# Optimization experiments

Measured on AMD Instinct MI355X. Metric: run time of the kernel, lower is better.

Reference implementation:

```python
import jax, jax.numpy as jnp
import numpy as np

GAMMAS = jnp.array([2.7, 2.1, 2.4, 2.0, 3.0, 2.9, 3.0, 2.5, 2.1, 2.6, 2.0, 2.1, 2.7, 2.4, 2.2], dtype=jnp.float32)

B, NCLS, H, W = 32, 15, 256, 256
K, CREG = 500, 2


def setup_inputs() -> dict:
    key = jax.random.key(0)
    ks = jax.random.split(key, 6)
    pred = jax.random.uniform(ks[0], (B, NCLS, H, W), dtype=jnp.float32)
    gt = jax.random.uniform(ks[1], (B, NCLS, H, W), dtype=jnp.float32)
    output = jax.random.normal(ks[2], (B, CREG, H, W), dtype=jnp.float32)
    mask = jax.random.randint(ks[3], (B, K), 0, 2, dtype=jnp.int32)
    ind = jax.random.randint(ks[4], (B, K), 0, H * W)
    target = jax.random.normal(ks[5], (B, K, CREG), dtype=jnp.float32)
    inde = jax.random.randint(jax.random.fold_in(key, 7), (B, K, 3), 0, 15)
    return {"pred": pred, "gt": gt, "output": output, "mask": mask,
            "ind": ind, "target": target, "inde": inde}


def _forward(pred, gt, output, mask, ind, target, inde):
    b, c_out = output.shape[0], output.shape[1]
    k = ind.shape[1]
    # _tranpose_and_gather_feat: [B,C,H,W] -> [B,HW,C], gather along dim 1
    feat = jnp.transpose(output, (0, 2, 3, 1)).reshape(b, -1, c_out)
    pre = jnp.take_along_axis(feat, ind[:, :, None].astype(jnp.int32), axis=1)  # [B,K,C]

    d = pre - target
    ad = jnp.abs(d)
    huber = jnp.where(ad < 1.0, 0.5 * d * d, ad - 0.5)
    l_bk = huber.mean(axis=2)  # [B,K]

    pos_mask = mask.astype(bool)
    factor = jnp.arctan(l_bk) * (2.0 / jnp.pi)
    vals = jnp.where(pos_mask, factor, 1.0).reshape(-1)

    b_idx = jnp.broadcast_to(jnp.arange(b)[:, None], (b, k)).reshape(-1)
    ch = inde[..., 0].reshape(-1)
    yy = inde[..., 1].reshape(-1)
    xx = inde[..., 2].reshape(-1)
    # in-place multiplicative scatter; torch's pred_uni aliases pred so the
    # modified tensor is used for BOTH pred_cat and pred_cat_uni below
    pred_mod = pred.at[b_idx, ch, yy, xx].multiply(vals)

    # loss is overwritten each loop iteration in the original: only the LAST
    # positive's smooth-L1 loss survives (0 if no positives)
    flat_m = pos_mask.reshape(-1)
    flat_l = l_bk.reshape(-1)
    last = jnp.max(jnp.where(flat_m, jnp.arange(flat_m.shape[0]), -1))
    loss0 = jnp.where(last >= 0, flat_l[jnp.clip(last, 0)], 0.0)

    # focal term, vectorized over the 15 class channels
    eps = 1e-12
    g = GAMMAS[None, :, None, None]
    pos_inds = (gt == 1.0).astype(pred.dtype)
    neg_inds = (gt < 1.0).astype(pred.dtype)
    neg_weights = jnp.power(1.0 - gt, 4)
    pos_loss = jnp.log(pred_mod + eps) * jnp.power(1.0 - pred_mod, g) * pos_inds
    neg_loss = jnp.log(1.0 - pred_mod + eps) * jnp.power(pred_mod, g) * neg_weights * neg_inds
    per_ch = jnp.sum(pos_loss + neg_loss, axis=(0, 2, 3))  # [15]
    loss = loss0 - jnp.sum(per_ch * GAMMAS * 0.5)

    num_pos = pos_inds.sum()
    return jnp.where(num_pos == 0, loss, loss / num_pos)


def reference(pred, gt, output, mask, ind, target, inde):
    return _forward(pred, gt, output, mask, ind, target, inde)
```

## Files before the change

### kernel.cpp

```cpp
#include <hip/hip_runtime.h>
#include <math.h>

#define BB 32
#define NCLS 15
#define HH 256
#define WW 256
#define KK 500
#define HW (HH*WW)
#define NELEM (BB*NCLS*HW)
#define N4 (NELEM/4)
#define NM (BB*NCLS*16*16)
#define BK (BB*KK)

#define MG 1536
#define MT 256
#define SPAN (MG*MT)
#define MITER 5

typedef float v4f __attribute__((ext_vector_type(4)));

#define OFF_LBK 4
#define OFF_M   16384

__constant__ float c_gammas[15] = {2.7f,2.1f,2.4f,2.0f,3.0f,2.9f,3.0f,2.5f,
                                   2.1f,2.6f,2.0f,2.1f,2.7f,2.4f,2.2f};

#define EXP2F(x) __builtin_amdgcn_exp2f(x)
#define LOG2F(x) __builtin_amdgcn_logf(x)
#define LN2 0.69314718055994530942f

__device__ __forceinline__ float elem(float p, float g, float gam, float& np) {
    float t    = 1.0f - g;
    float t2   = t * t;
    float negw = (g < 1.0f) ? t2 * t2 : 0.0f;
    float pw   = EXP2F(gam * LOG2F(p));
    float v    = (LN2 * LOG2F(1.0f - p + 1e-12f)) * pw * negw;
    if (g == 1.0f) {
        np += 1.0f;
        v += (LN2 * LOG2F(p + 1e-12f)) * EXP2F(gam * LOG2F(1.0f - p));
    }
    return v;
}

__device__ __forceinline__ float quad(v4f p, v4f g, int i, float& np) {
    int c = ((unsigned)i >> 14) % (unsigned)NCLS;
    float gam = c_gammas[c];
    return gam * (elem(p.x, g.x, gam, np) + elem(p.y, g.y, gam, np)
                + elem(p.z, g.z, gam, np) + elem(p.w, g.w, gam, np));
}

__device__ __forceinline__ float blockReduceSum(float v) {
    __shared__ float sh[4];
    #pragma unroll
    for (int o = 32; o > 0; o >>= 1) v += __shfl_down(v, o);
    int lane = threadIdx.x & 63, w = threadIdx.x >> 6;
    if (lane == 0) sh[w] = v;
    __syncthreads();
    float r = 0.0f;
    if (threadIdx.x == 0) r = sh[0] + sh[1] + sh[2] + sh[3];
    __syncthreads();
    return r;
}

__global__ __launch_bounds__(256) void k_init(float* ws) {
    int i = blockIdx.x * blockDim.x + threadIdx.x;
    if (i == 0) {
        ws[0] = 0.0f;
        ws[1] = 0.0f;
        ((int*)ws)[2] = -1;
        ((int*)ws)[3] = 0;
    }
    if (i < NM) ws[OFF_M + i] = 1.0f;
}

__global__ __launch_bounds__(256) void k_bk(const float* __restrict__ output,
                                            const int*   __restrict__ mask,
                                            const int*   __restrict__ ind,
                                            const float* __restrict__ target,
                                            const int*   __restrict__ inde,
                                            float* ws) {
    int t = blockIdx.x * blockDim.x + threadIdx.x;
    int lastv = -1;
    if (t < BK) {
        int b = t / KK;
        int pos = ind[t];
        const float* ob = output + (size_t)b * 2 * HW;
        float p0 = ob[pos];
        float p1 = ob[HW + pos];
        float d0 = p0 - target[t*2 + 0];
        float d1 = p1 - target[t*2 + 1];
        float a0 = fabsf(d0), a1 = fabsf(d1);
        float h0 = (a0 < 1.0f) ? 0.5f*d0*d0 : a0 - 0.5f;
        float h1 = (a1 < 1.0f) ? 0.5f*d1*d1 : a1 - 0.5f;
        float l  = 0.5f * (h0 + h1);
        ws[OFF_LBK + t] = l;
        if (mask[t] != 0) {
            lastv = t;
            float factor = atanf(l) * 0.63661977236758134308f;
            int ch = inde[t*3 + 0];
            int yy = inde[t*3 + 1];
            int xx = inde[t*3 + 2];
            int mi = ((b*NCLS + ch)*16 + yy)*16 + xx;
            unsigned int* addr = (unsigned int*)(ws + OFF_M + mi);
            unsigned int old = *addr, assumed;
            do {
                assumed = old;
                float nv = __uint_as_float(assumed) * factor;
                old = atomicCAS(addr, assumed, __float_as_uint(nv));
            } while (old != assumed);
        }
    }
    __shared__ int shm[4];
    int v = lastv;
    #pragma unroll
    for (int o = 32; o > 0; o >>= 1) v = max(v, __shfl_down(v, o));
    int lane = threadIdx.x & 63, w = threadIdx.x >> 6;
    if (lane == 0) shm[w] = v;
    __syncthreads();
    if (threadIdx.x == 0) {
        int m = max(max(shm[0], shm[1]), max(shm[2], shm[3]));
        if (m >= 0) atomicMax(((int*)ws) + 2, m);
    }
}

__global__ __launch_bounds__(256) void k_main(const v4f* __restrict__ pred,
                                              const v4f* __restrict__ gt,
                                              float* ws) {
    int t = blockIdx.x * MT + threadIdx.x;
    float acc = 0.0f, np = 0.0f;
    #pragma unroll 1
    for (int k = 0; k < MITER; ++k) {
        int i0 = t + k * 4 * SPAN;
        v4f p0 = __builtin_nontemporal_load(pred + i0);
        v4f p1 = __builtin_nontemporal_load(pred + i0 + SPAN);
        v4f p2 = __builtin_nontemporal_load(pred + i0 + 2*SPAN);
        v4f p3 = __builtin_nontemporal_load(pred + i0 + 3*SPAN);
        v4f g0 = __builtin_nontemporal_load(gt + i0);
        v4f g1 = __builtin_nontemporal_load(gt + i0 + SPAN);
        v4f g2 = __builtin_nontemporal_load(gt + i0 + 2*SPAN);
        v4f g3 = __builtin_nontemporal_load(gt + i0 + 3*SPAN);
        acc += quad(p0, g0, i0,          np);
        acc += quad(p1, g1, i0 + SPAN,   np);
        acc += quad(p2, g2, i0 + 2*SPAN, np);
        acc += quad(p3, g3, i0 + 3*SPAN, np);
    }
    float bs = blockReduceSum(acc);
    if (threadIdx.x == 0 && bs != 0.0f) atomicAdd(&ws[0], bs);
    float bn = blockReduceSum(np);
    if (threadIdx.x == 0 && bn != 0.0f) atomicAdd(&ws[1], bn);
}

__global__ __launch_bounds__(256) void k_corr(const float* __restrict__ pred,
                                              const float* __restrict__ gt,
                                              float* ws, float* out) {
    int i = blockIdx.x * blockDim.x + threadIdx.x;
    float acc = 0.0f, dummy = 0.0f;
    float m = ws[OFF_M + i];
    if (m != 1.0f) {
        int x  = i & 15;
        int y  = (i >> 4) & 15;
        int bc = i >> 8;
        int c  = bc % NCLS;
        size_t off = ((size_t)bc << 16) + (size_t)(y * WW + x);
        float p = pred[off];
        float g = gt[off];
        float gam = c_gammas[c];
        acc = gam * (elem(p * m, g, gam, dummy) - elem(p, g, gam, dummy));
    }
    float bs = blockReduceSum(acc);
    if (threadIdx.x == 0) {
        if (bs != 0.0f) atomicAdd(&ws[0], bs);
        __threadfence();
        int done = atomicAdd(((int*)ws) + 3, 1);
        if (done == gridDim.x - 1) {
            float S  = atomicAdd(&ws[0], 0.0f);
            float np = atomicAdd(&ws[1], 0.0f);
            int last = ((volatile int*)ws)[2];
            float loss0 = (last >= 0) ? ws[OFF_LBK + last] : 0.0f;
            float loss = loss0 - 0.5f * S;
            out[0] = (np == 0.0f) ? loss : loss / np;
        }
    }
}

extern "C" void kernel_launch(void* const* d_in, const int* in_sizes, int n_in,
                              void* d_out, int out_size, void* d_ws, size_t ws_size,
                              hipStream_t stream) {
    const float* pred   = (const float*)d_in[0];
    const float* gt     = (const float*)d_in[1];
    const float* output = (const float*)d_in[2];
    const int*   mask   = (const int*)d_in[3];
    const int*   ind    = (const int*)d_in[4];
    const float* target = (const float*)d_in[5];
    const int*   inde   = (const int*)d_in[6];
    float* ws  = (float*)d_ws;
    float* out = (float*)d_out;

    k_init<<<(NM + 255)/256, 256, 0, stream>>>(ws);
    k_bk  <<<(BK + 255)/256, 256, 0, stream>>>(output, mask, ind, target, inde, ws);
    k_main<<<MG, MT, 0, stream>>>((const v4f*)pred, (const v4f*)gt, ws);
    k_corr<<<NM/256, 256, 0, stream>>>(pred, gt, ws, out);
}
```

Baseline: 289.8 us.

## Fuse regression gather kernel into focal-loss streaming kernel with per-block channel mapping

Merges the per-(b,k) smooth-L1/scatter kernel into the main focal-loss reduction kernel. Each block handles 9 (b,k) entries in its first threads, then streams a quarter of one (b,c) slab. Because the channel is fixed per block, the gamma lookup is hoisted out of the loop. This removes one kernel launch and its tail, but puts the atomic scatter work on the critical path of some waves.

```diff
diff --git a/kernel.cpp b/kernel.cpp
--- a/kernel.cpp
+++ b/kernel.cpp
@@ -12,10 +12,11 @@
 #define NM (BB*NCLS*16*16)
 #define BK (BB*KK)
 
-#define MG 1536
-#define MT 256
-#define SPAN (MG*MT)
-#define MITER 5
+#define FG 1920
+#define FT 256
+#define SLAB4 16384
+#define QUART 4096
+#define BKPB 9
 
 typedef float v4f __attribute__((ext_vector_type(4)));
 
@@ -42,11 +43,9 @@
     return v;
 }
 
-__device__ __forceinline__ float quad(v4f p, v4f g, int i, float& np) {
-    int c = ((unsigned)i >> 14) % (unsigned)NCLS;
-    float gam = c_gammas[c];
-    return gam * (elem(p.x, g.x, gam, np) + elem(p.y, g.y, gam, np)
-                + elem(p.z, g.z, gam, np) + elem(p.w, g.w, gam, np));
+__device__ __forceinline__ float elem4(v4f p, v4f g, float gam, float& np) {
+    return elem(p.x, g.x, gam, np) + elem(p.y, g.y, gam, np)
+         + elem(p.z, g.z, gam, np) + elem(p.w, g.w, gam, np);
 }
 
 __device__ __forceinline__ float blockReduceSum(float v) {
@@ -73,81 +72,82 @@
     if (i < NM) ws[OFF_M + i] = 1.0f;
 }
 
-__global__ __launch_bounds__(256) void k_bk(const float* __restrict__ output,
-                                            const int*   __restrict__ mask,
-                                            const int*   __restrict__ ind,
-                                            const float* __restrict__ target,
-                                            const int*   __restrict__ inde,
-                                            float* ws) {
-    int t = blockIdx.x * blockDim.x + threadIdx.x;
+__global__ __launch_bounds__(256) void k_fused(const v4f*   __restrict__ pred,
+                                               const v4f*   __restrict__ gt,
+                                               const float* __restrict__ output,
+                                               const int*   __restrict__ mask,
+                                               const int*   __restrict__ ind,
+                                               const float* __restrict__ target,
+                                               const int*   __restrict__ inde,
+                                               float* ws) {
+    const int tid = threadIdx.x;
+    const int blk = blockIdx.x;
+
     int lastv = -1;
-    if (t < BK) {
-        int b = t / KK;
-        int pos = ind[t];
-        const float* ob = output + (size_t)b * 2 * HW;
-        float p0 = ob[pos];
-        float p1 = ob[HW + pos];
-        float d0 = p0 - target[t*2 + 0];
-        float d1 = p1 - target[t*2 + 1];
-        float a0 = fabsf(d0), a1 = fabsf(d1);
-        float h0 = (a0 < 1.0f) ? 0.5f*d0*d0 : a0 - 0.5f;
-        float h1 = (a1 < 1.0f) ? 0.5f*d1*d1 : a1 - 0.5f;
-        float l  = 0.5f * (h0 + h1);
-        ws[OFF_LBK + t] = l;
-        if (mask[t] != 0) {
-            lastv = t;
-            float factor = atanf(l) * 0.63661977236758134308f;
-            int ch = inde[t*3 + 0];
-            int yy = inde[t*3 + 1];
-            int xx = inde[t*3 + 2];
-            int mi = ((b*NCLS + ch)*16 + yy)*16 + xx;
-            unsigned int* addr = (unsigned int*)(ws + OFF_M + mi);
-            unsigned int old = *addr, assumed;
-            do {
-                assumed = old;
-                float nv = __uint_as_float(assumed) * factor;
-                old = atomicCAS(addr, assumed, __float_as_uint(nv));
-            } while (old != assumed);
+    if (tid < BKPB) {
+        int t = blk * BKPB + tid;
+        if (t < BK) {
+            int b = t / KK;
+            int pos = ind[t];
+            const float* ob = output + (size_t)b * 2 * HW;
+            float p0 = ob[pos];
+            float p1 = ob[HW + pos];
+            float d0 = p0 - target[t*2 + 0];
+            float d1 = p1 - target[t*2 + 1];
+            float a0 = fabsf(d0), a1 = fabsf(d1);
+            float h0 = (a0 < 1.0f) ? 0.5f*d0*d0 : a0 - 0.5f;
+            float h1 = (a1 < 1.0f) ? 0.5f*d1*d1 : a1 - 0.5f;
+            float l  = 0.5f * (h0 + h1);
+            ws[OFF_LBK + t] = l;
+            if (mask[t] != 0) {
+                lastv = t;
+                float factor = atanf(l) * 0.63661977236758134308f;
+                int ch = inde[t*3 + 0];
+                int yy = inde[t*3 + 1];
+                int xx = inde[t*3 + 2];
+                int mi = ((b*NCLS + ch)*16 + yy)*16 + xx;
+                unsigned int* addr = (unsigned int*)(ws + OFF_M + mi);
+                unsigned int old = *addr, assumed;
+                do {
+                    assumed = old;
+                    float nv = __uint_as_float(assumed) * factor;
+                    old = atomicCAS(addr, assumed, __float_as_uint(nv));
+                } while (old != assumed);
+            }
         }
     }
-    __shared__ int shm[4];
-    int v = lastv;
     #pragma unroll
-    for (int o = 32; o > 0; o >>= 1) v = max(v, __shfl_down(v, o));
-    int lane = threadIdx.x & 63, w = threadIdx.x >> 6;
-    if (lane == 0) shm[w] = v;
-    __syncthreads();
-    if (threadIdx.x == 0) {
-        int m = max(max(shm[0], shm[1]), max(shm[2], shm[3]));
-        if (m >= 0) atomicMax(((int*)ws) + 2, m);
-    }
-}
-
-__global__ __launch_bounds__(256) void k_main(const v4f* __restrict__ pred,
-                                              const v4f* __restrict__ gt,
-                                              float* ws) {
-    int t = blockIdx.x * MT + threadIdx.x;
+    for (int o = 8; o > 0; o >>= 1) lastv = max(lastv, __shfl_down(lastv, o));
+    if (tid == 0 && lastv >= 0) atomicMax(((int*)ws) + 2, lastv);
+
+    const int slab = blk >> 2;
+    const int c    = slab % NCLS;
+    const float gam = c_gammas[c];
+    const int base = slab * SLAB4 + (blk & 3) * QUART + tid;
+
     float acc = 0.0f, np = 0.0f;
     #pragma unroll 1
-    for (int k = 0; k < MITER; ++k) {
-        int i0 = t + k * 4 * SPAN;
+    for (int k = 0; k < 4; ++k) {
+        int i0 = base + k * 1024;
         v4f p0 = __builtin_nontemporal_load(pred + i0);
-        v4f p1 = __builtin_nontemporal_load(pred + i0 + SPAN);
-        v4f p2 = __builtin_nontemporal_load(pred + i0 + 2*SPAN);
-        v4f p3 = __builtin_nontemporal_load(pred + i0 + 3*SPAN);
-        v4f g0 = __builtin_nontemporal_load(gt + i0);
-        v4f g1 = __builtin_nontemporal_load(gt + i0 + SPAN);
-        v4f g2 = __builtin_nontemporal_load(gt + i0 + 2*SPAN);
-        v4f g3 = __builtin_nontemporal_load(gt + i0 + 3*SPAN);
-        acc += quad(p0, g0, i0,          np);
-        acc += quad(p1, g1, i0 + SPAN,   np);
-        acc += quad(p2, g2, i0 + 2*SPAN, np);
-        acc += quad(p3, g3, i0 + 3*SPAN, np);
-    }
+        v4f g0 = __builtin_nontemporal_load(gt   + i0);
+        v4f p1 = __builtin_nontemporal_load(pred + i0 + 256);
+        v4f g1 = __builtin_nontemporal_load(gt   + i0 + 256);
+        v4f p2 = __builtin_nontemporal_load(pred + i0 + 512);
+        v4f g2 = __builtin_nontemporal_load(gt   + i0 + 512);
+        v4f p3 = __builtin_nontemporal_load(pred + i0 + 768);
+        v4f g3 = __builtin_nontemporal_load(gt   + i0 + 768);
+        acc += elem4(p0, g0, gam, np);
+        acc += elem4(p1, g1, gam, np);
+        acc += elem4(p2, g2, gam, np);
+        acc += elem4(p3, g3, gam, np);
+    }
+    acc *= gam;
+
     float bs = blockReduceSum(acc);
-    if (threadIdx.x == 0 && bs != 0.0f) atomicAdd(&ws[0], bs);
+    if (tid == 0 && bs != 0.0f) atomicAdd(&ws[0], bs);
     float bn = blockReduceSum(np);
-    if (threadIdx.x == 0 && bn != 0.0f) atomicAdd(&ws[1], bn);
+    if (tid == 0 && bn != 0.0f) atomicAdd(&ws[1], bn);
 }
 
 __global__ __launch_bounds__(256) void k_corr(const float* __restrict__ pred,
@@ -196,8 +196,8 @@
     float* ws  = (float*)d_ws;
     float* out = (float*)d_out;
 
-    k_init<<<(NM + 255)/256, 256, 0, stream>>>(ws);
-    k_bk  <<<(BK + 255)/256, 256, 0, stream>>>(output, mask, ind, target, inde, ws);
-    k_main<<<MG, MT, 0, stream>>>((const v4f*)pred, (const v4f*)gt, ws);
-    k_corr<<<NM/256, 256, 0, stream>>>(pred, gt, ws, out);
-}
+    k_init <<<(NM + 255)/256, 256, 0, stream>>>(ws);
+    k_fused<<<FG, FT, 0, stream>>>((const v4f*)pred, (const v4f*)gt,
+                                   output, mask, ind, target, inde, ws);
+    k_corr <<<NM/256, 256, 0, stream>>>(pred, gt, ws, out);
+}
```

Measured after the change: 294.4 us. No clear change (+1.6%).
